# Optimization experiments

Measured on AMD Instinct MI355X. Metric: run time of the kernel, lower is better.

## Reference

```python
import jax, jax.numpy as jnp
import numpy as np

N_E, E_DIM, N = 1024, 128, 262144


def setup_inputs() -> dict:
    key = jax.random.key(0)
    kx, kw = jax.random.split(key)
    x = jax.random.normal(kx, (N, E_DIM), dtype=jnp.float32)
    # nn.Embedding weight initialized uniform(-1/n_e, 1/n_e)
    W = jax.random.uniform(kw, (N_E, E_DIM), dtype=jnp.float32,
                           minval=-1.0 / N_E, maxval=1.0 / N_E)
    return {"x": x, "W": W}


def reference(x, W):
    # d[n, k] = ||x_n||^2 + ||W_k||^2 - 2 x_n . W_k   -> shape [N, n_e]
    d = (jnp.sum(x * x, axis=1, keepdims=True)
         + jnp.sum(W * W, axis=1)
         - 2.0 * jnp.matmul(x, W.T))
    min_indices = jnp.argmin(d, axis=1)          # [N] int
    z_q = jnp.take(W, min_indices, axis=0)       # [N, e_dim] gather
    return (z_q, min_indices)
```

## Files before the change

### kernel.cpp

```cpp
#include <hip/hip_runtime.h>

#define EDIM 128
#define NE   1024
#define TAU  7e-5f
#define CAPP 65536

typedef short v8s __attribute__((ext_vector_type(8)));
typedef float v4f __attribute__((ext_vector_type(4)));

__device__ inline unsigned bf16_rne(float f) {
    unsigned u = __float_as_uint(f);
    return (u + 0x7fffu + ((u >> 16) & 1u)) >> 16;
}
__device__ inline float bf16_tof(unsigned h) { return __uint_as_float(h << 16); }

__global__ void vq_prep(const float* __restrict__ W,
                        unsigned short* __restrict__ whi,
                        unsigned short* __restrict__ wlo,
                        float* __restrict__ Wt,
                        float* __restrict__ swsq_ws)
{
#pragma clang fp contract(off)
    const int t = blockIdx.x * 256 + threadIdx.x;
    for (int i = t; i < NE * EDIM; i += 32768) {
        float v = W[i];
        unsigned h = bf16_rne(v);
        whi[i] = (unsigned short)h;
        wlo[i] = (unsigned short)bf16_rne(v - bf16_tof(h));
        Wt[((i & (EDIM - 1)) << 10) | (i >> 7)] = v;
    }
    if (t < NE) {
        const float4* wr = reinterpret_cast<const float4*>(W) + (size_t)t * 32;
        float4 A = wr[0], B = wr[1];
        float r0 = A.x*A.x, r1 = A.y*A.y, r2 = A.z*A.z, r3 = A.w*A.w;
        float r4 = B.x*B.x, r5 = B.y*B.y, r6 = B.z*B.z, r7 = B.w*B.w;
        #pragma unroll
        for (int i = 2; i < 32; i += 2) {
            float4 C = wr[i], D = wr[i + 1];
            r0 += C.x*C.x; r1 += C.y*C.y; r2 += C.z*C.z; r3 += C.w*C.w;
            r4 += D.x*D.x; r5 += D.y*D.y; r6 += D.z*D.z; r7 += D.w*D.w;
        }
        swsq_ws[t] = ((r0 + r1) + (r2 + r3)) + ((r4 + r5) + (r6 + r7));
    }
}

union SMem {
    struct { unsigned short wt[2][2][2048]; float sswsq[NE]; } p1;
    struct { float4 scan[2048]; int sbest[128]; } p2;
};

__global__ __launch_bounds__(256, 3) void vq_mfma5(
    const float* __restrict__ x,
    const unsigned short* __restrict__ whi, const unsigned short* __restrict__ wlo,
    const float* __restrict__ W, const float* __restrict__ swsq_ws,
    float* __restrict__ zq, float* __restrict__ idxout,
    int* __restrict__ cnt_pair, int* __restrict__ cnt_full,
    int* __restrict__ plist, int* __restrict__ flist)
{
    __shared__ SMem sm;

    const int tid = threadIdx.x;
    const int wid = tid >> 6;
    const int l   = tid & 63;
    const int m   = l & 15;
    const int g   = l >> 4;
    const int kb  = g * 8;

    const long long row0 = (long long)blockIdx.x * 128;
    const float4* x4 = reinterpret_cast<const float4*>(x);
    const float4* W4 = reinterpret_cast<const float4*>(W);

    const int scode = tid >> 4;
    const int skk   = (tid & 15) * 8;
    const int dst   = scode * EDIM + (skk ^ ((scode & 7) << 3));
    const int swz   = (m & 7) << 3;

    reinterpret_cast<float4*>(sm.p1.sswsq)[tid] =
        reinterpret_cast<const float4*>(swsq_ws)[tid];

    {
        v8s h0 = *reinterpret_cast<const v8s*>(whi + tid * 8);
        v8s l0 = *reinterpret_cast<const v8s*>(wlo + tid * 8);
        *reinterpret_cast<v8s*>(&sm.p1.wt[0][0][dst]) = h0;
        *reinterpret_cast<v8s*>(&sm.p1.wt[0][1][dst]) = l0;
    }

    const long long rA0 = row0 + wid * 32 + m;
    const long long rA1 = rA0 + 16;
    v8s a0h[4], a0l[4], a1h[4], a1l[4];
    #pragma unroll
    for (int ks = 0; ks < 4; ++ks) {
        float4 p0 = x4[rA0 * 32 + ks * 8 + g * 2];
        float4 p1 = x4[rA0 * 32 + ks * 8 + g * 2 + 1];
        float4 q0 = x4[rA1 * 32 + ks * 8 + g * 2];
        float4 q1 = x4[rA1 * 32 + ks * 8 + g * 2 + 1];
        float vp[8] = {p0.x,p0.y,p0.z,p0.w,p1.x,p1.y,p1.z,p1.w};
        float vq[8] = {q0.x,q0.y,q0.z,q0.w,q1.x,q1.y,q1.z,q1.w};
        #pragma unroll
        for (int e = 0; e < 8; ++e) {
            unsigned h0 = bf16_rne(vp[e]);
            a0h[ks][e] = (short)h0;
            a0l[ks][e] = (short)bf16_rne(vp[e] - bf16_tof(h0));
            unsigned h1 = bf16_rne(vq[e]);
            a1h[ks][e] = (short)h1;
            a1l[ks][e] = (short)bf16_rne(vq[e] - bf16_tof(h1));
        }
    }
    __syncthreads();

    float best[8], sec[8]; int bk[8];
    #pragma unroll
    for (int r = 0; r < 8; ++r) { best[r] = 3.4e38f; sec[r] = 3.4e38f; bk[r] = 0; }

    #pragma unroll 1
    for (int t = 0; t < 64; ++t) {
        const int buf = t & 1;
        v8s hn, ln;
        if (t + 1 < 64) {
            hn = *reinterpret_cast<const v8s*>(whi + (t + 1) * 2048 + tid * 8);
            ln = *reinterpret_cast<const v8s*>(wlo + (t + 1) * 2048 + tid * 8);
        }

        v4f acc0 = {0.f,0.f,0.f,0.f}, acc1 = {0.f,0.f,0.f,0.f};
        #pragma unroll
        for (int ks = 0; ks < 4; ++ks) {
            v8s bh = *(const v8s*)&sm.p1.wt[buf][0][(m * EDIM + ks * 32 + kb) ^ swz];
            v8s bl = *(const v8s*)&sm.p1.wt[buf][1][(m * EDIM + ks * 32 + kb) ^ swz];
            acc0 = __builtin_amdgcn_mfma_f32_16x16x32_bf16(a0h[ks], bh, acc0, 0, 0, 0);
            acc0 = __builtin_amdgcn_mfma_f32_16x16x32_bf16(a0l[ks], bh, acc0, 0, 0, 0);
            acc0 = __builtin_amdgcn_mfma_f32_16x16x32_bf16(a0h[ks], bl, acc0, 0, 0, 0);
            acc1 = __builtin_amdgcn_mfma_f32_16x16x32_bf16(a1h[ks], bh, acc1, 0, 0, 0);
            acc1 = __builtin_amdgcn_mfma_f32_16x16x32_bf16(a1l[ks], bh, acc1, 0, 0, 0);
            acc1 = __builtin_amdgcn_mfma_f32_16x16x32_bf16(a1h[ks], bl, acc1, 0, 0, 0);
        }

        const int k = t * 16 + m;
        const float wk2 = sm.p1.sswsq[k];
        #pragma unroll
        for (int r = 0; r < 4; ++r) {
            float s0 = fmaf(-2.f, acc0[r], wk2);
            sec[r]  = fminf(sec[r], fmaxf(s0, best[r]));
            bk[r]   = (s0 < best[r]) ? k : bk[r];
            best[r] = fminf(best[r], s0);
            float s1 = fmaf(-2.f, acc1[r], wk2);
            sec[4+r]  = fminf(sec[4+r], fmaxf(s1, best[4+r]));
            bk[4+r]   = (s1 < best[4+r]) ? k : bk[4+r];
            best[4+r] = fminf(best[4+r], s1);
        }

        if (t + 1 < 64) {
            *reinterpret_cast<v8s*>(&sm.p1.wt[buf ^ 1][0][dst]) = hn;
            *reinterpret_cast<v8s*>(&sm.p1.wt[buf ^ 1][1][dst]) = ln;
        }
        __syncthreads();
    }

    #pragma unroll
    for (int r = 0; r < 8; ++r) {
        int rowL = wid * 32 + ((r >> 2) << 4) + (g << 2) + (r & 3);
        float4 e; e.x = best[r]; e.y = sec[r]; e.z = __int_as_float(bk[r]); e.w = 0.f;
        sm.p2.scan[rowL * 16 + m] = e;
    }
    __syncthreads();

    if (tid < 128) {
        float b1 = 3.4e38f; int k1 = 0x7fffffff;
        #pragma unroll 1
        for (int mm = 0; mm < 16; ++mm) {
            float4 e = sm.p2.scan[tid * 16 + mm];
            int kk = __float_as_int(e.z);
            if (e.x < b1 || (e.x == b1 && kk < k1)) { b1 = e.x; k1 = kk; }
        }
        const float th = b1 + TAU;
        int nb = 0; bool asec = false;
        float b2 = 3.4e38f; int k2 = 0x7fffffff;
        #pragma unroll 1
        for (int mm = 0; mm < 16; ++mm) {
            float4 e = sm.p2.scan[tid * 16 + mm];
            int kk = __float_as_int(e.z);
            nb  += (e.x <= th) ? 1 : 0;
            asec = asec || (e.y <= th);
            if (kk != k1 && (e.x < b2 || (e.x == b2 && kk < k2))) { b2 = e.x; k2 = kk; }
        }
        sm.p2.sbest[tid] = k1;
        idxout[row0 + tid] = (float)k1;
        const int row = (int)(row0 + tid);
        if (asec || nb > 2) {
            int s2 = atomicAdd(cnt_full, 1);
            flist[s2] = row;
        } else if (nb == 2) {
            int slot = atomicAdd(cnt_pair, 1);
            if (slot < CAPP) { plist[2 * slot] = row; plist[2 * slot + 1] = k2; }
            else { int s2 = atomicAdd(cnt_full, 1); flist[s2] = row; }
        }
    }
    __syncthreads();

    float4* zq4 = reinterpret_cast<float4*>(zq);
    for (int i = tid; i < 128 * 32; i += 256) {
        int r = i >> 5, c4 = i & 31;
        zq4[row0 * 32 + i] = W4[(size_t)sm.p2.sbest[r] * 32 + c4];
    }
}

__global__ __launch_bounds__(256, 8) void vq_pair5(
    const float* __restrict__ x, const float* __restrict__ W,
    const float* __restrict__ swsq_ws,
    float* __restrict__ zq, float* __restrict__ idxout,
    const int* __restrict__ cnt_pair, const int* __restrict__ plist)
{
#pragma clang fp contract(off)
    int n = *cnt_pair; if (n > CAPP) n = CAPP;
    const int gsz = gridDim.x * 256;
    for (int i = blockIdx.x * 256 + threadIdx.x; i < n; i += gsz) {
        const int row = plist[2 * i];
        const int k2  = plist[2 * i + 1];
        const int k1  = (int)idxout[row];
        const float4* xr4 = reinterpret_cast<const float4*>(x + (size_t)row * EDIM);
        float4 A = xr4[0], B = xr4[1];
        float r0 = A.x*A.x, r1 = A.y*A.y, r2 = A.z*A.z, r3 = A.w*A.w;
        float r4 = B.x*B.x, r5 = B.y*B.y, r6 = B.z*B.z, r7 = B.w*B.w;
        #pragma unroll
        for (int q = 2; q < 32; q += 2) {
            float4 C = xr4[q], D = xr4[q + 1];
            r0 += C.x*C.x; r1 += C.y*C.y; r2 += C.z*C.z; r3 += C.w*C.w;
            r4 += D.x*D.x; r5 += D.y*D.y; r6 += D.z*D.z; r7 += D.w*D.w;
        }
        float xxv = ((r0 + r1) + (r2 + r3)) + ((r4 + r5) + (r6 + r7));
        const float* xr = x + (size_t)row * EDIM;
        const float* w1 = W + (size_t)k1 * EDIM;
        const float* w2 = W + (size_t)k2 * EDIM;
        float dot1 = 0.f, dot2 = 0.f;
        #pragma unroll 4
        for (int j = 0; j < EDIM; ++j) {
            float a = xr[j];
            dot1 = fmaf(a, w1[j], dot1);
            dot2 = fmaf(a, w2[j], dot2);
        }
        float d1 = (xxv + swsq_ws[k1]) - (dot1 + dot1);
        float d2 = (xxv + swsq_ws[k2]) - (dot2 + dot2);
        int kw = (d2 < d1 || (d2 == d1 && k2 < k1)) ? k2 : k1;
        if (kw != k1) {
            idxout[row] = (float)kw;
            const float4* wr = reinterpret_cast<const float4*>(W) + (size_t)kw * 32;
            float4* zr = reinterpret_cast<float4*>(zq) + (size_t)row * 32;
            #pragma unroll
            for (int q = 0; q < 32; ++q) zr[q] = wr[q];
        }
    }
}

__global__ __launch_bounds__(256, 4) void vq_full5(
    const float* __restrict__ x, const float* __restrict__ Wt,
    const float* __restrict__ W, const float* __restrict__ swsq_ws,
    float* __restrict__ zq, float* __restrict__ idxout,
    const int* __restrict__ cnt_full, const int* __restrict__ flist)
{
#pragma clang fp contract(off)
    const int nf = *cnt_full;
    const int lane = threadIdx.x & 63;
    const int nw = gridDim.x * 4;
    const float4* Wt4 = reinterpret_cast<const float4*>(Wt);
    const float4* W4  = reinterpret_cast<const float4*>(W);
    float4* zq4 = reinterpret_cast<float4*>(zq);

    for (int i = blockIdx.x * 4 + (threadIdx.x >> 6); i < nf; i += nw) {
        const long long row = flist[i];
        const float4* xr4 = reinterpret_cast<const float4*>(x + row * EDIM);
        float xxv;
        {
            float4 A = xr4[0], B = xr4[1];
            float r0 = A.x*A.x, r1 = A.y*A.y, r2 = A.z*A.z, r3 = A.w*A.w;
            float r4 = B.x*B.x, r5 = B.y*B.y, r6 = B.z*B.z, r7 = B.w*B.w;
            #pragma unroll
            for (int q = 2; q < 32; q += 2) {
                float4 C = xr4[q], D = xr4[q + 1];
                r0 += C.x*C.x; r1 += C.y*C.y; r2 += C.z*C.z; r3 += C.w*C.w;
                r4 += D.x*D.x; r5 += D.y*D.y; r6 += D.z*D.z; r7 += D.w*D.w;
            }
            xxv = ((r0 + r1) + (r2 + r3)) + ((r4 + r5) + (r6 + r7));
        }
        float acc[4][4];
        #pragma unroll
        for (int c = 0; c < 4; ++c)
            #pragma unroll
            for (int e = 0; e < 4; ++e) acc[c][e] = 0.f;
        const float* xr = x + row * EDIM;
        #pragma unroll 4
        for (int j = 0; j < EDIM; ++j) {
            float a = xr[j];
            #pragma unroll
            for (int c = 0; c < 4; ++c) {
                float4 w = Wt4[(size_t)j * 256 + c * 64 + lane];
                acc[c][0] = fmaf(a, w.x, acc[c][0]);
                acc[c][1] = fmaf(a, w.y, acc[c][1]);
                acc[c][2] = fmaf(a, w.z, acc[c][2]);
                acc[c][3] = fmaf(a, w.w, acc[c][3]);
            }
        }
        float dbest = 3.4e38f; int bkk = 0;
        #pragma unroll
        for (int c = 0; c < 4; ++c)
            #pragma unroll
            for (int e = 0; e < 4; ++e) {
                int k = c * 256 + lane * 4 + e;
                float t1 = xxv + swsq_ws[k];
                float d  = t1 - (acc[c][e] + acc[c][e]);
                if (d < dbest) { dbest = d; bkk = k; }
            }
        #pragma unroll
        for (int mk = 1; mk < 64; mk <<= 1) {
            float od = __shfl_xor(dbest, mk);
            int   ok = __shfl_xor(bkk, mk);
            if (od < dbest || (od == dbest && ok < bkk)) { dbest = od; bkk = ok; }
        }
        if (lane == 0) idxout[row] = (float)bkk;
        if (lane < 32) zq4[row * 32 + lane] = W4[(size_t)bkk * 32 + lane];
    }
}

__global__ __launch_bounds__(64, 2) void vq_v4(
    const float* __restrict__ x, const float* __restrict__ W,
    float* __restrict__ zq, float* __restrict__ idxout)
{
#pragma clang fp contract(off)
    __shared__ float swsq[NE];
    __shared__ int   sbest[64];
    const int tid = threadIdx.x;
    const long long row0 = (long long)blockIdx.x * 64;
    const long long row  = row0 + tid;
    const float4* x4 = reinterpret_cast<const float4*>(x);
    const float4* W4 = reinterpret_cast<const float4*>(W);
    float4 xr[32];
    #pragma unroll
    for (int i = 0; i < 32; ++i) xr[i] = x4[row * 32 + i];
    #pragma unroll
    for (int i = 0; i < 32; ++i)
        asm volatile("" : "+v"(xr[i].x), "+v"(xr[i].y), "+v"(xr[i].z), "+v"(xr[i].w));
    for (int k = tid; k < NE; k += 64) {
        const float4* wr = W4 + (size_t)k * 32;
        float4 A = wr[0], B = wr[1];
        float r0 = A.x*A.x, r1 = A.y*A.y, r2 = A.z*A.z, r3 = A.w*A.w;
        float r4 = B.x*B.x, r5 = B.y*B.y, r6 = B.z*B.z, r7 = B.w*B.w;
        #pragma unroll
        for (int i = 2; i < 32; i += 2) {
            float4 C = wr[i], D = wr[i + 1];
            r0 += C.x*C.x; r1 += C.y*C.y; r2 += C.z*C.z; r3 += C.w*C.w;
            r4 += D.x*D.x; r5 += D.y*D.y; r6 += D.z*D.z; r7 += D.w*D.w;
        }
        swsq[k] = ((r0 + r1) + (r2 + r3)) + ((r4 + r5) + (r6 + r7));
    }
    float xxv;
    {
        float r0 = xr[0].x*xr[0].x, r1 = xr[0].y*xr[0].y;
        float r2 = xr[0].z*xr[0].z, r3 = xr[0].w*xr[0].w;
        float r4 = xr[1].x*xr[1].x, r5 = xr[1].y*xr[1].y;
        float r6 = xr[1].z*xr[1].z, r7 = xr[1].w*xr[1].w;
        #pragma unroll
        for (int i = 2; i < 32; i += 2) {
            r0 += xr[i].x*xr[i].x;     r1 += xr[i].y*xr[i].y;
            r2 += xr[i].z*xr[i].z;     r3 += xr[i].w*xr[i].w;
            r4 += xr[i+1].x*xr[i+1].x; r5 += xr[i+1].y*xr[i+1].y;
            r6 += xr[i+1].z*xr[i+1].z; r7 += xr[i+1].w*xr[i+1].w;
        }
        xxv = ((r0 + r1) + (r2 + r3)) + ((r4 + r5) + (r6 + r7));
    }
    __syncthreads();
    float dbest = 3.4e38f; int bestk = 0;
    #pragma unroll 1
    for (int k0 = 0; k0 < NE; k0 += 8) {
        float acc[8];
        #pragma unroll
        for (int c = 0; c < 8; ++c) acc[c] = 0.f;
        #pragma unroll
        for (int j4 = 0; j4 < 32; ++j4) {
            const float4 a = xr[j4];
            #pragma unroll
            for (int c = 0; c < 8; ++c) {
                float4 w = W4[(size_t)(k0 + c) * 32 + j4];
                acc[c] = fmaf(a.x, w.x, acc[c]); acc[c] = fmaf(a.y, w.y, acc[c]);
                acc[c] = fmaf(a.z, w.z, acc[c]); acc[c] = fmaf(a.w, w.w, acc[c]);
            }
        }
        #pragma unroll
        for (int c = 0; c < 8; ++c) {
            float t1 = xxv + swsq[k0 + c];
            float d  = t1 - (acc[c] + acc[c]);
            if (d < dbest) { dbest = d; bestk = k0 + c; }
        }
    }
    sbest[tid] = bestk;
    idxout[row] = (float)bestk;
    __syncthreads();
    float4* zq4 = reinterpret_cast<float4*>(zq);
    for (int i = tid; i < 64 * 32; i += 64) {
        int r = i >> 5, c4 = i & 31;
        zq4[row0 * 32 + i] = W4[(size_t)sbest[r] * 32 + c4];
    }
}

extern "C" void kernel_launch(void* const* d_in, const int* in_sizes, int n_in,
                              void* d_out, int out_size, void* d_ws, size_t ws_size,
                              hipStream_t stream) {
    (void)n_in; (void)out_size;
    const float* x = (const float*)d_in[0];
    const float* W = (const float*)d_in[1];
    const int Nrows = in_sizes[0] / EDIM;

    float* zqp    = (float*)d_out;
    float* idxout = zqp + (size_t)Nrows * EDIM;

    const size_t need = 16 + 2 * (size_t)NE * EDIM * 2 + NE * 4
                      + (size_t)NE * EDIM * 4 + (size_t)CAPP * 2 * 4
                      + (size_t)Nrows * 4;
    if (ws_size < need) {
        vq_v4<<<dim3(Nrows / 64), dim3(64), 0, stream>>>(x, W, zqp, idxout);
        return;
    }

    char* p = (char*)d_ws;
    int*            cnt_pair = (int*)p;
    int*            cnt_full = (int*)(p + 4);
    unsigned short* whi   = (unsigned short*)(p + 16);
    unsigned short* wlo   = whi + NE * EDIM;
    float*          swsqw = (float*)(wlo + NE * EDIM);
    float*          Wt    = swsqw + NE;
    int*            plist = (int*)(Wt + NE * EDIM);
    int*            flist = plist + CAPP * 2;

    hipMemsetAsync(d_ws, 0, 16, stream);
    vq_prep<<<dim3(128), dim3(256), 0, stream>>>(W, whi, wlo, Wt, swsqw);
    vq_mfma5<<<dim3(Nrows / 128), dim3(256), 0, stream>>>(x, whi, wlo, W, swsqw,
                                                          zqp, idxout,
                                                          cnt_pair, cnt_full,
                                                          plist, flist);
    vq_pair5<<<dim3(256), dim3(256), 0, stream>>>(x, W, swsqw, zqp, idxout,
                                                  cnt_pair, plist);
    vq_full5<<<dim3(512), dim3(256), 0, stream>>>(x, Wt, W, swsqw, zqp, idxout,
                                                  cnt_full, flist);
}
```

Baseline: 395.7 us.

## Fold codebook norm into MFMA accumulator init and tune occupancy and prep

The accumulators are seeded with -0.5*||w_k||^2, so the score loop works directly on the dot product with max-tracking instead of applying an fma per element. Launch bounds go from 3 to 4 blocks per SM, and MFMA priority is raised around the matrix section. The prep kernel now uses twice as many blocks with coalesced transpose writes, and the final scan reads are staggered to reduce LDS bank conflicts. Scaling back by -2 at the end can change rounding near the tie threshold, and the higher occupancy target may cause register spills.

```diff
diff --git a/kernel.cpp b/kernel.cpp
--- a/kernel.cpp
+++ b/kernel.cpp
@@ -22,12 +22,14 @@
 {
 #pragma clang fp contract(off)
     const int t = blockIdx.x * 256 + threadIdx.x;
-    for (int i = t; i < NE * EDIM; i += 32768) {
+    #pragma unroll
+    for (int rep = 0; rep < 2; ++rep) {
+        int i = t + rep * 65536;
         float v = W[i];
         unsigned h = bf16_rne(v);
         whi[i] = (unsigned short)h;
         wlo[i] = (unsigned short)bf16_rne(v - bf16_tof(h));
-        Wt[((i & (EDIM - 1)) << 10) | (i >> 7)] = v;
+        Wt[i] = W[(i & 1023) * EDIM + (i >> 10)];
     }
     if (t < NE) {
         const float4* wr = reinterpret_cast<const float4*>(W) + (size_t)t * 32;
@@ -45,11 +47,11 @@
 }
 
 union SMem {
-    struct { unsigned short wt[2][2][2048]; float sswsq[NE]; } p1;
+    struct { unsigned short wt[2][2][2048]; float snwk2h[NE]; } p1;
     struct { float4 scan[2048]; int sbest[128]; } p2;
 };
 
-__global__ __launch_bounds__(256, 3) void vq_mfma5(
+__global__ __launch_bounds__(256, 4) void vq_mfma6(
     const float* __restrict__ x,
     const unsigned short* __restrict__ whi, const unsigned short* __restrict__ wlo,
     const float* __restrict__ W, const float* __restrict__ swsq_ws,
@@ -75,8 +77,11 @@
     const int dst   = scode * EDIM + (skk ^ ((scode & 7) << 3));
     const int swz   = (m & 7) << 3;
 
-    reinterpret_cast<float4*>(sm.p1.sswsq)[tid] =
-        reinterpret_cast<const float4*>(swsq_ws)[tid];
+    {
+        float4 v = reinterpret_cast<const float4*>(swsq_ws)[tid];
+        v.x *= -0.5f; v.y *= -0.5f; v.z *= -0.5f; v.w *= -0.5f;
+        reinterpret_cast<float4*>(sm.p1.snwk2h)[tid] = v;
+    }
 
     {
         v8s h0 = *reinterpret_cast<const v8s*>(whi + tid * 8);
@@ -110,7 +115,7 @@
 
     float best[8], sec[8]; int bk[8];
     #pragma unroll
-    for (int r = 0; r < 8; ++r) { best[r] = 3.4e38f; sec[r] = 3.4e38f; bk[r] = 0; }
+    for (int r = 0; r < 8; ++r) { best[r] = -3.4e38f; sec[r] = -3.4e38f; bk[r] = 0; }
 
     #pragma unroll 1
     for (int t = 0; t < 64; ++t) {
@@ -121,7 +126,11 @@
             ln = *reinterpret_cast<const v8s*>(wlo + (t + 1) * 2048 + tid * 8);
         }
 
-        v4f acc0 = {0.f,0.f,0.f,0.f}, acc1 = {0.f,0.f,0.f,0.f};
+        const int k = t * 16 + m;
+        const float h = sm.p1.snwk2h[k];
+        v4f acc0 = {h, h, h, h};
+        v4f acc1 = {h, h, h, h};
+        __builtin_amdgcn_s_setprio(1);
         #pragma unroll
         for (int ks = 0; ks < 4; ++ks) {
             v8s bh = *(const v8s*)&sm.p1.wt[buf][0][(m * EDIM + ks * 32 + kb) ^ swz];
@@ -133,19 +142,18 @@
             acc1 = __builtin_amdgcn_mfma_f32_16x16x32_bf16(a1l[ks], bh, acc1, 0, 0, 0);
             acc1 = __builtin_amdgcn_mfma_f32_16x16x32_bf16(a1h[ks], bl, acc1, 0, 0, 0);
         }
-
-        const int k = t * 16 + m;
-        const float wk2 = sm.p1.sswsq[k];
+        __builtin_amdgcn_s_setprio(0);
+
         #pragma unroll
         for (int r = 0; r < 4; ++r) {
-            float s0 = fmaf(-2.f, acc0[r], wk2);
-            sec[r]  = fminf(sec[r], fmaxf(s0, best[r]));
-            bk[r]   = (s0 < best[r]) ? k : bk[r];
-            best[r] = fminf(best[r], s0);
-            float s1 = fmaf(-2.f, acc1[r], wk2);
-            sec[4+r]  = fminf(sec[4+r], fmaxf(s1, best[4+r]));
-            bk[4+r]   = (s1 < best[4+r]) ? k : bk[4+r];
-            best[4+r] = fminf(best[4+r], s1);
+            float a0r = acc0[r];
+            sec[r]  = fmaxf(sec[r], fminf(a0r, best[r]));
+            bk[r]   = (a0r > best[r]) ? k : bk[r];
+            best[r] = fmaxf(best[r], a0r);
+            float a1r = acc1[r];
+            sec[4+r]  = fmaxf(sec[4+r], fminf(a1r, best[4+r]));
+            bk[4+r]   = (a1r > best[4+r]) ? k : bk[4+r];
+            best[4+r] = fmaxf(best[4+r], a1r);
         }
 
         if (t + 1 < 64) {
@@ -158,16 +166,20 @@
     #pragma unroll
     for (int r = 0; r < 8; ++r) {
         int rowL = wid * 32 + ((r >> 2) << 4) + (g << 2) + (r & 3);
-        float4 e; e.x = best[r]; e.y = sec[r]; e.z = __int_as_float(bk[r]); e.w = 0.f;
+        float4 e;
+        e.x = -2.f * best[r]; e.y = -2.f * sec[r];
+        e.z = __int_as_float(bk[r]); e.w = 0.f;
         sm.p2.scan[rowL * 16 + m] = e;
     }
     __syncthreads();
 
     if (tid < 128) {
+        const int stag = tid & 7;
         float b1 = 3.4e38f; int k1 = 0x7fffffff;
         #pragma unroll 1
         for (int mm = 0; mm < 16; ++mm) {
-            float4 e = sm.p2.scan[tid * 16 + mm];
+            int mme = mm ^ stag;
+            float4 e = sm.p2.scan[tid * 16 + mme];
             int kk = __float_as_int(e.z);
             if (e.x < b1 || (e.x == b1 && kk < k1)) { b1 = e.x; k1 = kk; }
         }
@@ -176,7 +188,8 @@
         float b2 = 3.4e38f; int k2 = 0x7fffffff;
         #pragma unroll 1
         for (int mm = 0; mm < 16; ++mm) {
-            float4 e = sm.p2.scan[tid * 16 + mm];
+            int mme = mm ^ stag;
+            float4 e = sm.p2.scan[tid * 16 + mme];
             int kk = __float_as_int(e.z);
             nb  += (e.x <= th) ? 1 : 0;
             asec = asec || (e.y <= th);
@@ -429,8 +442,8 @@
     int*            flist = plist + CAPP * 2;
 
     hipMemsetAsync(d_ws, 0, 16, stream);
-    vq_prep<<<dim3(128), dim3(256), 0, stream>>>(W, whi, wlo, Wt, swsqw);
-    vq_mfma5<<<dim3(Nrows / 128), dim3(256), 0, stream>>>(x, whi, wlo, W, swsqw,
+    vq_prep<<<dim3(256), dim3(256), 0, stream>>>(W, whi, wlo, Wt, swsqw);
+    vq_mfma6<<<dim3(Nrows / 128), dim3(256), 0, stream>>>(x, whi, wlo, W, swsqw,
                                                           zqp, idxout,
                                                           cnt_pair, cnt_full,
                                                           plist, flist);
```

New measurement: 533.1 us. 1.35x slower.
